# Kernel optimization log

Hardware: AMD Instinct MI355X
Metric: run time of the kernel (lower is better)

The kernel has to match this reference:

```python
import jax, jax.numpy as jnp
import numpy as np

EMBED = 1024
HEADS = 16
HD = EMBED // HEADS
FF = 4096
EPS = 1e-5

def _layernorm(x, g, b):
    mu = jnp.mean(x, axis=-1, keepdims=True)
    var = jnp.mean(jnp.square(x - mu), axis=-1, keepdims=True)
    return (x - mu) * jax.lax.rsqrt(var + EPS) * g + b

def setup_inputs() -> dict:
    key = jax.random.key(0)
    ks = jax.random.split(key, 10)
    s = 0.02
    return {
        "x": jax.random.normal(ks[0], (4, 2048, EMBED), dtype=jnp.float32),
        "Wq": jax.random.normal(ks[1], (EMBED, EMBED), dtype=jnp.float32) * s,
        "Wk": jax.random.normal(ks[2], (EMBED, EMBED), dtype=jnp.float32) * s,
        "Wv": jax.random.normal(ks[3], (EMBED, EMBED), dtype=jnp.float32) * s,
        "Wo": jax.random.normal(ks[4], (EMBED, EMBED), dtype=jnp.float32) * s,
        "bo": jnp.zeros((EMBED,), dtype=jnp.float32),
        "W1": jax.random.normal(ks[5], (EMBED, FF), dtype=jnp.float32) * s,
        "b1": jnp.zeros((FF,), dtype=jnp.float32),
        "W2": jax.random.normal(ks[6], (FF, EMBED), dtype=jnp.float32) * s,
        "b2": jnp.zeros((EMBED,), dtype=jnp.float32),
        "g1": jnp.ones((EMBED,), dtype=jnp.float32),
        "be1": jnp.zeros((EMBED,), dtype=jnp.float32),
        "g2": jnp.ones((EMBED,), dtype=jnp.float32),
        "be2": jnp.zeros((EMBED,), dtype=jnp.float32),
    }

def reference(x, Wq, Wk, Wv, Wo, bo, W1, b1, W2, b2, g1, be1, g2, be2):
    B, T, _ = x.shape
    # --- pre-norm self-attention (dropout = identity in eval) ---
    h = _layernorm(x, g1, be1)
    q = (h @ Wq).reshape(B, T, HEADS, HD).transpose(0, 2, 1, 3)  # bhtd
    k = (h @ Wk).reshape(B, T, HEADS, HD).transpose(0, 2, 1, 3)
    v = (h @ Wv).reshape(B, T, HEADS, HD).transpose(0, 2, 1, 3)
    scores = jnp.einsum('bhid,bhjd->bhij', q, k) / jnp.sqrt(jnp.float32(HD))
    causal = jnp.tril(jnp.ones((T, T), dtype=bool))
    scores = jnp.where(causal[None, None], scores, -jnp.inf)
    attn = jax.nn.softmax(scores, axis=-1)
    out = jnp.einsum('bhij,bhjd->bhid', attn, v)
    out = out.transpose(0, 2, 1, 3).reshape(B, T, EMBED)
    out = out @ Wo + bo
    x = x + out
    # --- pre-norm GELU FFN ---
    h2 = _layernorm(x, g2, be2)
    ff = jax.nn.gelu(h2 @ W1 + b1, approximate=False) @ W2 + b2
    return x + ff
```

## Files before the change

### kernel.cpp

```cpp
#include <hip/hip_runtime.h>

typedef unsigned short u16;
typedef __attribute__((ext_vector_type(8))) short bf16x8;
typedef __attribute__((ext_vector_type(4))) float f32x4;

#define EMBED 1024
#define FFDIM 4096
#define SEQ   2048
#define NTOK  8192
#define ATT_C 0.18033688011112042f

__device__ __forceinline__ u16 f2bf(float f) {
  union { float f; unsigned int u; } c; c.f = f;
  unsigned int r = ((c.u >> 16) & 1u) + 0x7fffu;
  return (u16)((c.u + r) >> 16);
}

__device__ __forceinline__ unsigned cvtpk(float lo, float hi) {
  unsigned r;
  asm("v_cvt_pk_bf16_f32 %0, %1, %2" : "=v"(r) : "v"(lo), "v"(hi));
  return r;
}

__device__ __forceinline__ void gload16(const u16* g, u16* l) {
  __builtin_amdgcn_global_load_lds((const __attribute__((address_space(1))) void*)g,
                                   (__attribute__((address_space(3))) void*)l, 16, 0, 0);
}

__global__ __launch_bounds__(256) void wtrans(const float* __restrict__ W,
                                              u16* __restrict__ Wt, int K, int N) {
  __shared__ float tile[32][33];
  const int tx = threadIdx.x & 31, ty = threadIdx.x >> 5;
  const int n0 = blockIdx.x << 5, k0 = blockIdx.y << 5;
#pragma unroll
  for (int r = 0; r < 32; r += 8)
    tile[ty + r][tx] = W[(size_t)(k0 + ty + r) * N + n0 + tx];
  __syncthreads();
#pragma unroll
  for (int r = 0; r < 32; r += 8)
    Wt[(size_t)(n0 + ty + r) * K + k0 + tx] = f2bf(tile[tx][ty + r]);
}

__global__ __launch_bounds__(256) void vtrans(const u16* __restrict__ qkv,
                                              u16* __restrict__ Vt) {
  __shared__ u16 tile[32][33];
  const int tx = threadIdx.x & 31, ty = threadIdx.x >> 5;
  const int t0 = blockIdx.x << 5;
  const int rg0 = blockIdx.y << 5;
  const int bh = rg0 >> 6, d0 = rg0 & 63;
  const int b = bh >> 4, h = bh & 15;
#pragma unroll
  for (int r = 0; r < 32; r += 8)
    tile[ty + r][tx] = qkv[(size_t)(b * SEQ + t0 + ty + r) * 3072 + 2048 + h * 64 + d0 + tx];
  __syncthreads();
#pragma unroll
  for (int r = 0; r < 32; r += 8)
    Vt[(size_t)(rg0 + ty + r) * SEQ + t0 + tx] = tile[tx][ty + r];
}

__global__ __launch_bounds__(256) void ln_kernel(const float* __restrict__ xin,
                                                 const float* __restrict__ gamma,
                                                 const float* __restrict__ beta,
                                                 u16* __restrict__ out) {
  const int row = blockIdx.x, tid = threadIdx.x;
  const float4 v = reinterpret_cast<const float4*>(xin + (size_t)row * EMBED)[tid];
  float s  = v.x + v.y + v.z + v.w;
  float ss = v.x * v.x + v.y * v.y + v.z * v.z + v.w * v.w;
#pragma unroll
  for (int m = 1; m < 64; m <<= 1) { s += __shfl_xor(s, m); ss += __shfl_xor(ss, m); }
  __shared__ float red[8];
  if ((tid & 63) == 0) { red[tid >> 6] = s; red[4 + (tid >> 6)] = ss; }
  __syncthreads();
  s  = red[0] + red[1] + red[2] + red[3];
  ss = red[4] + red[5] + red[6] + red[7];
  const float mean = s * (1.0f / EMBED);
  const float var  = ss * (1.0f / EMBED) - mean * mean;
  const float rstd = rsqrtf(var + 1e-5f);
  const float4 g  = reinterpret_cast<const float4*>(gamma)[tid];
  const float4 bb = reinterpret_cast<const float4*>(beta)[tid];
  ushort4 o;
  o.x = f2bf((v.x - mean) * rstd * g.x + bb.x);
  o.y = f2bf((v.y - mean) * rstd * g.y + bb.y);
  o.z = f2bf((v.z - mean) * rstd * g.z + bb.z);
  o.w = f2bf((v.w - mean) * rstd * g.w + bb.w);
  reinterpret_cast<ushort4*>(out + (size_t)row * EMBED)[tid] = o;
}

template <int EPI>
__global__ __launch_bounds__(256) void gemm_bt(const u16* __restrict__ A,
                                               const u16* __restrict__ Bt,
                                               void* __restrict__ Cv,
                                               const float* __restrict__ bias,
                                               const float* __restrict__ res,
                                               int M, int N, int K) {
  __shared__ __align__(16) u16 As[128 * 64];
  __shared__ __align__(16) u16 Bs[128 * 64];
  const int tid = threadIdx.x;
  const int lane = tid & 63, wid = tid >> 6;
  const int l4 = lane >> 4, l15 = lane & 15;
  const int wr = wid >> 1, wc = wid & 1;
  const int brow = blockIdx.y << 7, bcol = blockIdx.x << 7;

  const f32x4 z4 = {0.f, 0.f, 0.f, 0.f};
  f32x4 acc[4][4];
#pragma unroll
  for (int m = 0; m < 4; ++m)
#pragma unroll
    for (int n = 0; n < 4; ++n) acc[m][n] = z4;

  const int srow = tid >> 3;
  const int srck = ((tid & 7) << 4) ^ ((srow & 7) << 4);
  const u16* gA = A  + (size_t)(brow + srow) * K + (srck >> 1);
  const u16* gB = Bt + (size_t)(bcol + srow) * K + (srck >> 1);

  const int nk = K >> 6;
  for (int kt = 0; kt < nk; ++kt) {
    __syncthreads();
#pragma unroll
    for (int p = 0; p < 4; ++p) {
      gload16(gA + (size_t)p * 32 * K, &As[(p * 256 + wid * 64) * 8]);
      gload16(gB + (size_t)p * 32 * K, &Bs[(p * 256 + wid * 64) * 8]);
    }
    gA += 64; gB += 64;
    __syncthreads();
#pragma unroll
    for (int ks = 0; ks < 2; ++ks) {
      bf16x8 af[4], bfr[4];
      const int kk = ks * 32 + (l4 << 3);
#pragma unroll
      for (int m = 0; m < 4; ++m) {
        const int r = wr * 64 + m * 16 + l15;
        af[m] = *(const bf16x8*)&As[r * 64 + (kk ^ ((r & 7) << 3))];
      }
#pragma unroll
      for (int n = 0; n < 4; ++n) {
        const int r = wc * 64 + n * 16 + l15;
        bfr[n] = *(const bf16x8*)&Bs[r * 64 + (kk ^ ((r & 7) << 3))];
      }
#pragma unroll
      for (int m = 0; m < 4; ++m)
#pragma unroll
        for (int n = 0; n < 4; ++n)
          acc[m][n] = __builtin_amdgcn_mfma_f32_16x16x32_bf16(af[m], bfr[n], acc[m][n], 0, 0, 0);
    }
  }

  const int rowb = brow + wr * 64 + (l4 << 2);
  const int colb = bcol + wc * 64 + l15;
#pragma unroll
  for (int n = 0; n < 4; ++n) {
    const int col = colb + n * 16;
    float bv = 0.f;
    if (EPI != 0) bv = bias[col];
#pragma unroll
    for (int m = 0; m < 4; ++m) {
#pragma unroll
      for (int j = 0; j < 4; ++j) {
        const int row = rowb + m * 16 + j;
        const float v = acc[m][n][j];
        if (EPI == 0) {
          ((u16*)Cv)[(size_t)row * N + col] = f2bf(v);
        } else if (EPI == 1) {
          ((float*)Cv)[(size_t)row * N + col] = v + bv + res[(size_t)row * N + col];
        } else {
          const float t = v + bv;
          const float gl = 0.5f * t * (1.0f + erff(t * 0.70710678118654752f));
          ((u16*)Cv)[(size_t)row * N + col] = f2bf(gl);
        }
      }
    }
  }
}

__global__ __launch_bounds__(256) void attn_fwd(const u16* __restrict__ qkv,
                                                const u16* __restrict__ Vt,
                                                u16* __restrict__ attn) {
  __shared__ __align__(16) u16 Ks[64 * 72];
  __shared__ __align__(16) u16 Vs[64 * 72];
  __shared__ __align__(16) u16 Ps[4 * 32 * 72];
  const int tid = threadIdx.x, lane = tid & 63, wid = tid >> 6;
  const int l4 = lane >> 4, l15 = lane & 15;
  const int bh = blockIdx.y, b = bh >> 4, h = bh & 15;
  const size_t bt0 = (size_t)b * SEQ;
  u16* Pw = &Ps[wid * 32 * 72];

  const int sr = tid >> 2;
  const int sc0 = (tid & 3) << 4;
  const u16* kbase = qkv + bt0 * 3072 + 1024 + h * 64;
  const u16* vbase = Vt + (size_t)bh * 64 * SEQ;
  const f32x4 z4 = {0.f, 0.f, 0.f, 0.f};

#pragma unroll
  for (int ph = 0; ph < 2; ++ph) {
    const int Qb = ((ph == 0) ? (int)blockIdx.x : 15 - (int)blockIdx.x) << 7;
    const int qw = Qb + wid * 32;

    bf16x8 aq[2][2];
#pragma unroll
    for (int qt = 0; qt < 2; ++qt) {
      const u16* qp = qkv + (bt0 + qw + qt * 16 + l15) * 3072 + h * 64 + (l4 << 3);
      aq[qt][0] = *(const bf16x8*)qp;
      aq[qt][1] = *(const bf16x8*)(qp + 32);
    }

    f32x4 o[2][4];
#pragma unroll
    for (int qt = 0; qt < 2; ++qt)
#pragma unroll
      for (int dt = 0; dt < 4; ++dt) o[qt][dt] = z4;
    float mrun[2] = {-1e30f, -1e30f}, lrun[2] = {0.f, 0.f};

    bf16x8 kp0 = *(const bf16x8*)(kbase + (size_t)sr * 3072 + sc0);
    bf16x8 kp1 = *(const bf16x8*)(kbase + (size_t)sr * 3072 + sc0 + 8);
    bf16x8 vp0 = *(const bf16x8*)(vbase + (size_t)sr * SEQ + sc0);
    bf16x8 vp1 = *(const bf16x8*)(vbase + (size_t)sr * SEQ + sc0 + 8);

    const int jend = Qb + 128;
    for (int j0 = 0; j0 < jend; j0 += 64) {
      __syncthreads();
      *(bf16x8*)&Ks[sr * 72 + sc0]     = kp0;
      *(bf16x8*)&Ks[sr * 72 + sc0 + 8] = kp1;
      *(bf16x8*)&Vs[sr * 72 + sc0]     = vp0;
      *(bf16x8*)&Vs[sr * 72 + sc0 + 8] = vp1;
      __syncthreads();

      if (j0 + 64 < jend) {
        const size_t kro = (size_t)(j0 + 64 + sr);
        kp0 = *(const bf16x8*)(kbase + kro * 3072 + sc0);
        kp1 = *(const bf16x8*)(kbase + kro * 3072 + sc0 + 8);
        vp0 = *(const bf16x8*)(vbase + (size_t)sr * SEQ + j0 + 64 + sc0);
        vp1 = *(const bf16x8*)(vbase + (size_t)sr * SEQ + j0 + 64 + sc0 + 8);
      }

      if (j0 > qw + 31) continue;

#pragma unroll
      for (int qt = 0; qt < 2; ++qt) {
        const int qhi = qw + qt * 16 + 15;
        if (j0 > qhi) continue;
        const int nt = min(4, ((qhi - j0) >> 4) + 1);
        const int qrow = qhi - 15 + l15;

        f32x4 s[4];
#pragma unroll
        for (int t = 0; t < 4; ++t) {
          if (t < nt) {
            const bf16x8 ak0 = *(const bf16x8*)&Ks[(t * 16 + l15) * 72 + (l4 << 3)];
            const bf16x8 ak1 = *(const bf16x8*)&Ks[(t * 16 + l15) * 72 + 32 + (l4 << 3)];
            f32x4 a = z4;
            a = __builtin_amdgcn_mfma_f32_16x16x32_bf16(ak0, aq[qt][0], a, 0, 0, 0);
            a = __builtin_amdgcn_mfma_f32_16x16x32_bf16(ak1, aq[qt][1], a, 0, 0, 0);
            s[t] = a;
          }
        }

        float mt = -1e30f;
#pragma unroll
        for (int t = 0; t < 4; ++t) {
          if (t < nt) {
            if (j0 + t * 16 + 15 > qhi - 15) {
              const int kvb = j0 + t * 16 + (l4 << 2);
#pragma unroll
              for (int j = 0; j < 4; ++j)
                if (kvb + j > qrow) s[t][j] = -1e30f;
            }
#pragma unroll
            for (int j = 0; j < 4; ++j) mt = fmaxf(mt, s[t][j]);
          }
        }
        mt = fmaxf(mt, __shfl_xor(mt, 16));
        mt = fmaxf(mt, __shfl_xor(mt, 32));
        const float mn = fmaxf(mrun[qt], mt);
        const float mnc = mn * ATT_C;
        const float sc = exp2f(mrun[qt] * ATT_C - mnc);
        mrun[qt] = mn;

        float ls = 0.f;
        uint2 pw[4];
#pragma unroll
        for (int t = 0; t < 4; ++t) {
          if (t < nt) {
            const float p0 = exp2f(__builtin_fmaf(s[t][0], ATT_C, -mnc));
            const float p1 = exp2f(__builtin_fmaf(s[t][1], ATT_C, -mnc));
            const float p2 = exp2f(__builtin_fmaf(s[t][2], ATT_C, -mnc));
            const float p3 = exp2f(__builtin_fmaf(s[t][3], ATT_C, -mnc));
            ls += (p0 + p1) + (p2 + p3);
            pw[t].x = cvtpk(p0, p1);
            pw[t].y = cvtpk(p2, p3);
          } else {
            pw[t].x = 0u; pw[t].y = 0u;
          }
        }
#pragma unroll
        for (int t = 0; t < 4; ++t)
          *(uint2*)&Pw[(qt * 16 + l15) * 72 + t * 16 + (l4 << 2)] = pw[t];

        ls += __shfl_xor(ls, 16);
        ls += __shfl_xor(ls, 32);
        lrun[qt] = lrun[qt] * sc + ls;

#pragma unroll
        for (int dt = 0; dt < 4; ++dt)
#pragma unroll
          for (int j = 0; j < 4; ++j) o[qt][dt][j] *= sc;

        const int nc = (nt + 1) >> 1;
#pragma unroll
        for (int c = 0; c < 2; ++c) {
          if (c < nc) {
            const bf16x8 ap = *(const bf16x8*)&Pw[(qt * 16 + l15) * 72 + c * 32 + (l4 << 3)];
#pragma unroll
            for (int dt = 0; dt < 4; ++dt) {
              const bf16x8 bv = *(const bf16x8*)&Vs[(dt * 16 + l15) * 72 + c * 32 + (l4 << 3)];
              o[qt][dt] = __builtin_amdgcn_mfma_f32_16x16x32_bf16(bv, ap, o[qt][dt], 0, 0, 0);
            }
          }
        }
      }
    }

#pragma unroll
    for (int qt = 0; qt < 2; ++qt) {
      const float rl = 1.0f / lrun[qt];
#pragma unroll
      for (int dt = 0; dt < 4; ++dt) {
        uint2 w;
        w.x = cvtpk(o[qt][dt][0] * rl, o[qt][dt][1] * rl);
        w.y = cvtpk(o[qt][dt][2] * rl, o[qt][dt][3] * rl);
        *(uint2*)&Pw[(qt * 16 + l15) * 72 + dt * 16 + (l4 << 2)] = w;
      }
    }
#pragma unroll
    for (int rep = 0; rep < 4; ++rep) {
      const int unit = rep * 64 + lane;
      const int r = unit >> 3, c = unit & 7;
      const bf16x8 v = *(const bf16x8*)&Pw[r * 72 + c * 8];
      *(bf16x8*)&attn[(bt0 + qw + r) * EMBED + h * 64 + c * 8] = v;
    }
  }
}

extern "C" void kernel_launch(void* const* d_in, const int* in_sizes, int n_in,
                              void* d_out, int out_size, void* d_ws, size_t ws_size,
                              hipStream_t stream) {
  const float* x   = (const float*)d_in[0];
  const float* Wq  = (const float*)d_in[1];
  const float* Wk  = (const float*)d_in[2];
  const float* Wv  = (const float*)d_in[3];
  const float* Wo  = (const float*)d_in[4];
  const float* bo  = (const float*)d_in[5];
  const float* W1  = (const float*)d_in[6];
  const float* b1  = (const float*)d_in[7];
  const float* W2  = (const float*)d_in[8];
  const float* b2  = (const float*)d_in[9];
  const float* g1  = (const float*)d_in[10];
  const float* be1 = (const float*)d_in[11];
  const float* g2  = (const float*)d_in[12];
  const float* be2 = (const float*)d_in[13];

  char* ws = (char*)d_ws;
  u16* wqkv_t = (u16*)(ws + 0);
  u16* wo_t   = (u16*)(ws + 6291456);
  u16* w1_t   = (u16*)(ws + 8388608);
  u16* w2_t   = (u16*)(ws + 16777216);
  u16* hbuf   = (u16*)(ws + 25165824);
  u16* qkv    = (u16*)(ws + 41943040);
  u16* ff1    = (u16*)(ws + 41943040);
  u16* vt     = (u16*)(ws + 92274688);
  u16* attnb  = (u16*)(ws + 109051904);
  float* x2   = (float*)(ws + 125829120);
  float* outp = (float*)d_out;

  dim3 blk(256);
  wtrans<<<dim3(32, 32),  blk, 0, stream>>>(Wq, wqkv_t,               1024, 1024);
  wtrans<<<dim3(32, 32),  blk, 0, stream>>>(Wk, wqkv_t + 1024 * 1024, 1024, 1024);
  wtrans<<<dim3(32, 32),  blk, 0, stream>>>(Wv, wqkv_t + 2048 * 1024, 1024, 1024);
  wtrans<<<dim3(32, 32),  blk, 0, stream>>>(Wo, wo_t,                 1024, 1024);
  wtrans<<<dim3(128, 32), blk, 0, stream>>>(W1, w1_t,                 1024, 4096);
  wtrans<<<dim3(32, 128), blk, 0, stream>>>(W2, w2_t,                 4096, 1024);

  ln_kernel<<<dim3(8192), blk, 0, stream>>>(x, g1, be1, hbuf);
  gemm_bt<0><<<dim3(24, 64), blk, 0, stream>>>(hbuf, wqkv_t, qkv, nullptr, nullptr,
                                               8192, 3072, 1024);
  vtrans<<<dim3(64, 128), blk, 0, stream>>>(qkv, vt);
  attn_fwd<<<dim3(8, 64), blk, 0, stream>>>(qkv, vt, attnb);
  gemm_bt<1><<<dim3(8, 64), blk, 0, stream>>>(attnb, wo_t, x2, bo, x,
                                              8192, 1024, 1024);
  ln_kernel<<<dim3(8192), blk, 0, stream>>>(x2, g2, be2, hbuf);
  gemm_bt<2><<<dim3(32, 64), blk, 0, stream>>>(hbuf, w1_t, ff1, b1, nullptr,
                                               8192, 4096, 1024);
  gemm_bt<1><<<dim3(8, 64), blk, 0, stream>>>(ff1, w2_t, outp, b2, x2,
                                              8192, 1024, 4096);
}
```

Measured before the change: 473.9 us.

## Use 8 waves per attention block, lazy softmax rescale, XCD-swizzled GEMM tiles

The attention kernel now runs 512 threads per block, with each wave owning 16 query rows instead of 32. This halves per-wave register state and raises occupancy, and the K/V staging work is spread across more threads. A lazy rescale skips the running-max update and the output rescale when the new tile max stays within a threshold of the current max, which trims exp and multiply work but risks precision if the threshold is too large. The GEMM remaps block indices so consecutive workgroups land on the same XCD chiplet, aiming to improve L2 reuse.

```diff
diff --git a/kernel.cpp b/kernel.cpp
--- a/kernel.cpp
+++ b/kernel.cpp
@@ -99,7 +99,13 @@
   const int lane = tid & 63, wid = tid >> 6;
   const int l4 = lane >> 4, l15 = lane & 15;
   const int wr = wid >> 1, wc = wid & 1;
-  const int brow = blockIdx.y << 7, bcol = blockIdx.x << 7;
+
+  const int gx = gridDim.x;
+  const int nwg = gx * gridDim.y;
+  const int flat = (int)blockIdx.y * gx + (int)blockIdx.x;
+  const int cpx = nwg >> 3;
+  const int swz = (flat & 7) * cpx + (flat >> 3);
+  const int brow = (swz / gx) << 7, bcol = (swz % gx) << 7;
 
   const f32x4 z4 = {0.f, 0.f, 0.f, 0.f};
   f32x4 acc[4][4];
@@ -172,20 +178,20 @@
   }
 }
 
-__global__ __launch_bounds__(256) void attn_fwd(const u16* __restrict__ qkv,
+__global__ __launch_bounds__(512) void attn_fwd(const u16* __restrict__ qkv,
                                                 const u16* __restrict__ Vt,
                                                 u16* __restrict__ attn) {
   __shared__ __align__(16) u16 Ks[64 * 72];
   __shared__ __align__(16) u16 Vs[64 * 72];
-  __shared__ __align__(16) u16 Ps[4 * 32 * 72];
+  __shared__ __align__(16) u16 Ps[8 * 16 * 72];
   const int tid = threadIdx.x, lane = tid & 63, wid = tid >> 6;
   const int l4 = lane >> 4, l15 = lane & 15;
   const int bh = blockIdx.y, b = bh >> 4, h = bh & 15;
   const size_t bt0 = (size_t)b * SEQ;
-  u16* Pw = &Ps[wid * 32 * 72];
-
-  const int sr = tid >> 2;
-  const int sc0 = (tid & 3) << 4;
+  u16* Pw = &Ps[wid * 16 * 72];
+
+  const int sr = tid >> 3;
+  const int sc0 = (tid & 7) << 3;
   const u16* kbase = qkv + bt0 * 3072 + 1024 + h * 64;
   const u16* vbase = Vt + (size_t)bh * 64 * SEQ;
   const f32x4 z4 = {0.f, 0.f, 0.f, 0.f};
@@ -193,145 +199,131 @@
 #pragma unroll
   for (int ph = 0; ph < 2; ++ph) {
     const int Qb = ((ph == 0) ? (int)blockIdx.x : 15 - (int)blockIdx.x) << 7;
-    const int qw = Qb + wid * 32;
-
-    bf16x8 aq[2][2];
-#pragma unroll
-    for (int qt = 0; qt < 2; ++qt) {
-      const u16* qp = qkv + (bt0 + qw + qt * 16 + l15) * 3072 + h * 64 + (l4 << 3);
-      aq[qt][0] = *(const bf16x8*)qp;
-      aq[qt][1] = *(const bf16x8*)(qp + 32);
-    }
-
-    f32x4 o[2][4];
-#pragma unroll
-    for (int qt = 0; qt < 2; ++qt)
-#pragma unroll
-      for (int dt = 0; dt < 4; ++dt) o[qt][dt] = z4;
-    float mrun[2] = {-1e30f, -1e30f}, lrun[2] = {0.f, 0.f};
-
-    bf16x8 kp0 = *(const bf16x8*)(kbase + (size_t)sr * 3072 + sc0);
-    bf16x8 kp1 = *(const bf16x8*)(kbase + (size_t)sr * 3072 + sc0 + 8);
-    bf16x8 vp0 = *(const bf16x8*)(vbase + (size_t)sr * SEQ + sc0);
-    bf16x8 vp1 = *(const bf16x8*)(vbase + (size_t)sr * SEQ + sc0 + 8);
+    const int qw = Qb + wid * 16;
+    const int qlane = qw + l15;
+
+    const u16* qp = qkv + (bt0 + qlane) * 3072 + h * 64 + (l4 << 3);
+    const bf16x8 aq0 = *(const bf16x8*)qp;
+    const bf16x8 aq1 = *(const bf16x8*)(qp + 32);
+
+    f32x4 o[4];
+#pragma unroll
+    for (int dt = 0; dt < 4; ++dt) o[dt] = z4;
+    float mrun = -1e30f, lrun = 0.f;
+
+    bf16x8 kp = *(const bf16x8*)(kbase + (size_t)sr * 3072 + sc0);
+    bf16x8 vp = *(const bf16x8*)(vbase + (size_t)sr * SEQ + sc0);
 
     const int jend = Qb + 128;
     for (int j0 = 0; j0 < jend; j0 += 64) {
       __syncthreads();
-      *(bf16x8*)&Ks[sr * 72 + sc0]     = kp0;
-      *(bf16x8*)&Ks[sr * 72 + sc0 + 8] = kp1;
-      *(bf16x8*)&Vs[sr * 72 + sc0]     = vp0;
-      *(bf16x8*)&Vs[sr * 72 + sc0 + 8] = vp1;
+      *(bf16x8*)&Ks[sr * 72 + sc0] = kp;
+      *(bf16x8*)&Vs[sr * 72 + sc0] = vp;
       __syncthreads();
 
       if (j0 + 64 < jend) {
-        const size_t kro = (size_t)(j0 + 64 + sr);
-        kp0 = *(const bf16x8*)(kbase + kro * 3072 + sc0);
-        kp1 = *(const bf16x8*)(kbase + kro * 3072 + sc0 + 8);
-        vp0 = *(const bf16x8*)(vbase + (size_t)sr * SEQ + j0 + 64 + sc0);
-        vp1 = *(const bf16x8*)(vbase + (size_t)sr * SEQ + j0 + 64 + sc0 + 8);
-      }
-
-      if (j0 > qw + 31) continue;
-
-#pragma unroll
-      for (int qt = 0; qt < 2; ++qt) {
-        const int qhi = qw + qt * 16 + 15;
-        if (j0 > qhi) continue;
-        const int nt = min(4, ((qhi - j0) >> 4) + 1);
-        const int qrow = qhi - 15 + l15;
-
-        f32x4 s[4];
-#pragma unroll
-        for (int t = 0; t < 4; ++t) {
-          if (t < nt) {
-            const bf16x8 ak0 = *(const bf16x8*)&Ks[(t * 16 + l15) * 72 + (l4 << 3)];
-            const bf16x8 ak1 = *(const bf16x8*)&Ks[(t * 16 + l15) * 72 + 32 + (l4 << 3)];
-            f32x4 a = z4;
-            a = __builtin_amdgcn_mfma_f32_16x16x32_bf16(ak0, aq[qt][0], a, 0, 0, 0);
-            a = __builtin_amdgcn_mfma_f32_16x16x32_bf16(ak1, aq[qt][1], a, 0, 0, 0);
-            s[t] = a;
+        kp = *(const bf16x8*)(kbase + (size_t)(j0 + 64 + sr) * 3072 + sc0);
+        vp = *(const bf16x8*)(vbase + (size_t)sr * SEQ + j0 + 64 + sc0);
+      }
+
+      if (j0 > qw + 15) continue;
+      const int nt = min(4, ((qw + 15 - j0) >> 4) + 1);
+
+      f32x4 s[4];
+#pragma unroll
+      for (int t = 0; t < 4; ++t) {
+        if (t < nt) {
+          const bf16x8 ak0 = *(const bf16x8*)&Ks[(t * 16 + l15) * 72 + (l4 << 3)];
+          const bf16x8 ak1 = *(const bf16x8*)&Ks[(t * 16 + l15) * 72 + 32 + (l4 << 3)];
+          f32x4 a = z4;
+          a = __builtin_amdgcn_mfma_f32_16x16x32_bf16(ak0, aq0, a, 0, 0, 0);
+          a = __builtin_amdgcn_mfma_f32_16x16x32_bf16(ak1, aq1, a, 0, 0, 0);
+          s[t] = a;
+        }
+      }
+
+      float mt = -1e30f;
+#pragma unroll
+      for (int t = 0; t < 4; ++t) {
+        if (t < nt) {
+          if (j0 + t * 16 + 15 > qw) {
+            const int kvb = j0 + t * 16 + (l4 << 2);
+#pragma unroll
+            for (int j = 0; j < 4; ++j)
+              if (kvb + j > qlane) s[t][j] = -1e30f;
           }
-        }
-
-        float mt = -1e30f;
-#pragma unroll
-        for (int t = 0; t < 4; ++t) {
-          if (t < nt) {
-            if (j0 + t * 16 + 15 > qhi - 15) {
-              const int kvb = j0 + t * 16 + (l4 << 2);
-#pragma unroll
-              for (int j = 0; j < 4; ++j)
-                if (kvb + j > qrow) s[t][j] = -1e30f;
-            }
-#pragma unroll
-            for (int j = 0; j < 4; ++j) mt = fmaxf(mt, s[t][j]);
+          mt = fmaxf(mt, fmaxf(fmaxf(s[t][0], s[t][1]), fmaxf(s[t][2], s[t][3])));
+        }
+      }
+      mt = fmaxf(mt, __shfl_xor(mt, 16));
+      mt = fmaxf(mt, __shfl_xor(mt, 32));
+
+      const bool skip = __all(mt <= mrun + 44.0f);
+      float scq = 1.0f;
+      if (!skip) {
+        const float mn = fmaxf(mrun, mt);
+        scq = exp2f((mrun - mn) * ATT_C);
+        mrun = mn;
+      }
+      const float mc = mrun * ATT_C;
+
+      float ls = 0.f;
+      uint2 pw[4];
+#pragma unroll
+      for (int t = 0; t < 4; ++t) {
+        if (t < nt) {
+          const float p0 = exp2f(__builtin_fmaf(s[t][0], ATT_C, -mc));
+          const float p1 = exp2f(__builtin_fmaf(s[t][1], ATT_C, -mc));
+          const float p2 = exp2f(__builtin_fmaf(s[t][2], ATT_C, -mc));
+          const float p3 = exp2f(__builtin_fmaf(s[t][3], ATT_C, -mc));
+          ls += (p0 + p1) + (p2 + p3);
+          pw[t].x = cvtpk(p0, p1);
+          pw[t].y = cvtpk(p2, p3);
+        } else {
+          pw[t].x = 0u; pw[t].y = 0u;
+        }
+      }
+#pragma unroll
+      for (int t = 0; t < 4; ++t)
+        *(uint2*)&Pw[l15 * 72 + t * 16 + (l4 << 2)] = pw[t];
+
+      ls += __shfl_xor(ls, 16);
+      ls += __shfl_xor(ls, 32);
+
+      if (!skip) {
+        lrun = lrun * scq + ls;
+#pragma unroll
+        for (int dt = 0; dt < 4; ++dt)
+#pragma unroll
+          for (int j = 0; j < 4; ++j) o[dt][j] *= scq;
+      } else {
+        lrun += ls;
+      }
+
+      const int nc = (nt + 1) >> 1;
+#pragma unroll
+      for (int c = 0; c < 2; ++c) {
+        if (c < nc) {
+          const bf16x8 ap = *(const bf16x8*)&Pw[l15 * 72 + c * 32 + (l4 << 3)];
+#pragma unroll
+          for (int dt = 0; dt < 4; ++dt) {
+            const bf16x8 bv = *(const bf16x8*)&Vs[(dt * 16 + l15) * 72 + c * 32 + (l4 << 3)];
+            o[dt] = __builtin_amdgcn_mfma_f32_16x16x32_bf16(bv, ap, o[dt], 0, 0, 0);
           }
         }
-        mt = fmaxf(mt, __shfl_xor(mt, 16));
-        mt = fmaxf(mt, __shfl_xor(mt, 32));
-        const float mn = fmaxf(mrun[qt], mt);
-        const float mnc = mn * ATT_C;
-        const float sc = exp2f(mrun[qt] * ATT_C - mnc);
-        mrun[qt] = mn;
-
-        float ls = 0.f;
-        uint2 pw[4];
-#pragma unroll
-        for (int t = 0; t < 4; ++t) {
-          if (t < nt) {
-            const float p0 = exp2f(__builtin_fmaf(s[t][0], ATT_C, -mnc));
-            const float p1 = exp2f(__builtin_fmaf(s[t][1], ATT_C, -mnc));
-            const float p2 = exp2f(__builtin_fmaf(s[t][2], ATT_C, -mnc));
-            const float p3 = exp2f(__builtin_fmaf(s[t][3], ATT_C, -mnc));
-            ls += (p0 + p1) + (p2 + p3);
-            pw[t].x = cvtpk(p0, p1);
-            pw[t].y = cvtpk(p2, p3);
-          } else {
-            pw[t].x = 0u; pw[t].y = 0u;
-          }
-        }
-#pragma unroll
-        for (int t = 0; t < 4; ++t)
-          *(uint2*)&Pw[(qt * 16 + l15) * 72 + t * 16 + (l4 << 2)] = pw[t];
-
-        ls += __shfl_xor(ls, 16);
-        ls += __shfl_xor(ls, 32);
-        lrun[qt] = lrun[qt] * sc + ls;
-
-#pragma unroll
-        for (int dt = 0; dt < 4; ++dt)
-#pragma unroll
-          for (int j = 0; j < 4; ++j) o[qt][dt][j] *= sc;
-
-        const int nc = (nt + 1) >> 1;
-#pragma unroll
-        for (int c = 0; c < 2; ++c) {
-          if (c < nc) {
-            const bf16x8 ap = *(const bf16x8*)&Pw[(qt * 16 + l15) * 72 + c * 32 + (l4 << 3)];
-#pragma unroll
-            for (int dt = 0; dt < 4; ++dt) {
-              const bf16x8 bv = *(const bf16x8*)&Vs[(dt * 16 + l15) * 72 + c * 32 + (l4 << 3)];
-              o[qt][dt] = __builtin_amdgcn_mfma_f32_16x16x32_bf16(bv, ap, o[qt][dt], 0, 0, 0);
-            }
-          }
-        }
-      }
-    }
-
-#pragma unroll
-    for (int qt = 0; qt < 2; ++qt) {
-      const float rl = 1.0f / lrun[qt];
-#pragma unroll
-      for (int dt = 0; dt < 4; ++dt) {
-        uint2 w;
-        w.x = cvtpk(o[qt][dt][0] * rl, o[qt][dt][1] * rl);
-        w.y = cvtpk(o[qt][dt][2] * rl, o[qt][dt][3] * rl);
-        *(uint2*)&Pw[(qt * 16 + l15) * 72 + dt * 16 + (l4 << 2)] = w;
-      }
-    }
-#pragma unroll
-    for (int rep = 0; rep < 4; ++rep) {
+      }
+    }
+
+    const float rl = 1.0f / lrun;
+#pragma unroll
+    for (int dt = 0; dt < 4; ++dt) {
+      uint2 w;
+      w.x = cvtpk(o[dt][0] * rl, o[dt][1] * rl);
+      w.y = cvtpk(o[dt][2] * rl, o[dt][3] * rl);
+      *(uint2*)&Pw[l15 * 72 + dt * 16 + (l4 << 2)] = w;
+    }
+#pragma unroll
+    for (int rep = 0; rep < 2; ++rep) {
       const int unit = rep * 64 + lane;
       const int r = unit >> 3, c = unit & 7;
       const bf16x8 v = *(const bf16x8*)&Pw[r * 72 + c * 8];
@@ -383,7 +375,7 @@
   gemm_bt<0><<<dim3(24, 64), blk, 0, stream>>>(hbuf, wqkv_t, qkv, nullptr, nullptr,
                                                8192, 3072, 1024);
   vtrans<<<dim3(64, 128), blk, 0, stream>>>(qkv, vt);
-  attn_fwd<<<dim3(8, 64), blk, 0, stream>>>(qkv, vt, attnb);
+  attn_fwd<<<dim3(8, 64), dim3(512), 0, stream>>>(qkv, vt, attnb);
   gemm_bt<1><<<dim3(8, 64), blk, 0, stream>>>(attnb, wo_t, x2, bo, x,
                                               8192, 1024, 1024);
   ln_kernel<<<dim3(8192), blk, 0, stream>>>(x2, g2, be2, hbuf);
```

Result: faster. 432.0 us (-8.8%).
